# Kernel tuning notes

Measured on AMD Instinct MI355X. Metric: run time of the kernel, lower is better.

The kernel has to match this reference:

```python
import jax, jax.numpy as jnp
import numpy as np

B, L, FD = 16, 196, 2048      # batch, fmap locations (14x14), resnet101 feat dim
N, WD, HD, DD = 1000, 300, 512, 5  # n_class, word_dim, hid_dim, d_dim
E, TMAX, NIMG = 50000, 5, 1000     # n_edges, gru steps, imagenet classes


def setup_inputs():
    key = jax.random.key(0)
    ks = jax.random.split(key, 32)
    p = lambda k, s: (jax.random.normal(k, s, jnp.float32) * 0.02)
    z = lambda n: jnp.zeros((n,), jnp.float32)
    return {
        'feats': jax.random.normal(ks[0], (B, L, FD), jnp.float32),
        'embed': jax.random.normal(ks[1], (N, WD), jnp.float32),
        'edges': jax.random.randint(ks[2], (2, E), 0, N, jnp.int32),
        # attention key/query nets
        'W_key': p(ks[3], (FD, HD)), 'b_key': z(HD),
        'W_query': p(ks[4], (WD, HD)), 'b_query': z(HD),
        # F_in: feat_dim -> 512 -> d_dim (relu)
        'Wf1': p(ks[5], (FD, 512)), 'bf1': z(512),
        'Wf2': p(ks[6], (512, DD)), 'bf2': z(DD),
        # F_rel: 2*word_dim -> 256 -> 1 (relu)
        'Wr1': p(ks[7], (2 * WD, 256)), 'br1': z(256),
        'Wr2': p(ks[8], (256, 1)), 'br2': z(1),
        # F_out: d_dim -> 512 -> 1 (relu)
        'Wo1': p(ks[9], (DD, 512)), 'bo1': z(512),
        'Wo2': p(ks[10], (512, 1)), 'bo2': z(1),
        # GRUCell (torch layout: [3*d, d] stacked r,z,n)
        'W_ih': p(ks[11], (3 * DD, DD)), 'b_ih': z(3 * DD),
        'W_hh': p(ks[12], (3 * DD, DD)), 'b_hh': z(3 * DD),
        # imagenet classifier on pooled features
        'W_clf': p(ks[13], (FD, NIMG)), 'b_clf': z(NIMG),
    }


def _gru_cell(x, h, W_ih, W_hh, b_ih, b_hh):
    gi = x @ W_ih.T + b_ih            # [M, 3d]
    gh = h @ W_hh.T + b_hh
    i_r, i_z, i_n = jnp.split(gi, 3, axis=-1)
    h_r, h_z, h_n = jnp.split(gh, 3, axis=-1)
    r = jax.nn.sigmoid(i_r + h_r)
    zg = jax.nn.sigmoid(i_z + h_z)
    n = jnp.tanh(i_n + r * h_n)
    return (1.0 - zg) * n + zg * h


def reference(feats, embed, edges, W_key, b_key, W_query, b_query,
              Wf1, bf1, Wf2, bf2, Wr1, br1, Wr2, br2, Wo1, bo1, Wo2, bo2,
              W_ih, b_ih, W_hh, b_hh, W_clf, b_clf):
    # imagenet scores from globally pooled backbone features
    pooled = jnp.mean(feats, axis=1)                      # [B, FD]
    imgnet_scores = jax.nn.softmax(pooled @ W_clf + b_clf, axis=1)

    # label-conditional spatial attention
    keys = feats @ W_key + b_key                          # [B, L, HD]
    queries = embed @ W_query + b_query                   # [N, HD]
    scores = jnp.einsum('blh,nh->bnl', keys, queries)     # [B, N, L]
    attn = jax.nn.softmax(scores, axis=2)
    graph_input = jnp.einsum('bnl,blf->bnf', attn, feats) # [B, N, FD]
    graph_input = graph_input.reshape(-1, FD)             # [B*N, FD]

    # F_in MLP -> initial hidden state
    h0 = jax.nn.relu(graph_input @ Wf1 + bf1) @ Wf2 + bf2  # [B*N, DD]

    # edge weights from word-embedding pairs, scattered into dense [N, N]
    et = jnp.concatenate([embed[edges[0]], embed[edges[1]]], axis=1)  # [E, 2*WD]
    vals = jnp.tanh((jax.nn.relu(et @ Wr1 + br1) @ Wr2 + br2).reshape(-1))
    prop_mat = jnp.zeros((N, N), jnp.float32).at[edges[0], edges[1]].add(vals)

    # t_max message-passing + GRU steps (sequential recurrence)
    def step(hidden, _):
        msg = jnp.tanh(jnp.einsum('nm,bmd->bnd', prop_mat,
                                  hidden.reshape(B, N, DD))).reshape(-1, DD)
        return _gru_cell(msg, hidden, W_ih, W_hh, b_ih, b_hh), None
    hidden, _ = jax.lax.scan(step, h0, None, length=TMAX)

    logits = (jax.nn.relu(hidden @ Wo1 + bo1) @ Wo2 + bo2).reshape(B, N)
    return logits, attn, imgnet_scores
```

## Files before the change

kernel.cpp:

```cpp
#include <hip/hip_runtime.h>
#include <hip/hip_bf16.h>
#include <math.h>

#define B_   16
#define L_   196
#define FD_  2048
#define N_   1000
#define WD_  300
#define HD_  512
#define DD_  5
#define E_   50000
#define TMAX_ 5
#define NIMG_ 1000
#define WDP_ 320
#define LP_  224
#define EKP_ 640

typedef __attribute__((ext_vector_type(8))) short bf16x8;
typedef __attribute__((ext_vector_type(4))) float f32x4;

#define SMEM_MEGA1    24832
#define SMEM_MM_SPLIT 24576
#define SMEM_MM_NS    12288
#define SMEM_PREP     4352

__device__ __forceinline__ short bf_hi(float x) {
    unsigned u = __float_as_uint(x);
    unsigned r = u + 0x7fffu + ((u >> 16) & 1u);
    return (short)(r >> 16);
}
__device__ __forceinline__ float bf2f_(short s) {
    return __uint_as_float(((unsigned)(unsigned short)s) << 16);
}

__device__ __forceinline__ void gl16(const short* g, char* l) {
    __builtin_amdgcn_global_load_lds(
        (const __attribute__((address_space(1))) void*)g,
        (__attribute__((address_space(3))) void*)l, 16, 0, 0);
}

#define OUT_SPLIT 1
#define OUT_SC    2
#define OUT_F1T   3
#define OUT_H0    4

template<int OUTMODE, bool SPLIT>
__device__ __forceinline__ void mm_core(
    char* sm, int bx, int by, int zb,
    const short* __restrict__ Ah, const short* __restrict__ Al,
    const short* __restrict__ Bh, const short* __restrict__ Bl,
    const float* __restrict__ bias, void* __restrict__ C0, void* __restrict__ C1,
    void* __restrict__ C2, const float* __restrict__ W2,
    int M, int N, int K, int kbeg, int kend)
{
    char* AsH = sm;
    char* AsL = sm + 8192;
    char* BsH = sm + (SPLIT ? 16384 : 8192);
    char* BsL = sm + 20480;
    int t = threadIdx.x;
    int lane = t & 63, w = t >> 6;
    int q = lane >> 4, r = lane & 15;
    int row0 = by * 128, col0 = bx * 64;

    int srow = t >> 2, cd = t & 3;
    int cg = cd ^ ((srow >> 1) & 3);
    int gA0 = row0 + srow;       if (gA0 >= M) gA0 = M - 1;
    int gA1 = row0 + 64 + srow;  if (gA1 >= M) gA1 = M - 1;
    int gB  = col0 + srow;       if (gB  >= N) gB  = N - 1;
    const short* pA0 = Ah + (long)gA0 * K + cg * 8 + kbeg;
    const short* pA1 = Ah + (long)gA1 * K + cg * 8 + kbeg;
    const short* pB  = Bh + (long)gB  * K + cg * 8 + kbeg;
    const short* pA0l = Ah; const short* pA1l = Ah; const short* pBl = Bh;
    if (SPLIT) {
        pA0l = Al + (long)gA0 * K + cg * 8 + kbeg;
        pA1l = Al + (long)gA1 * K + cg * 8 + kbeg;
        pBl  = Bl + (long)gB  * K + cg * 8 + kbeg;
    }
    char* dA0 = AsH + t * 16;
    char* dA1 = AsH + 4096 + t * 16;
    char* dB  = BsH + t * 16;
    char* dA0l = AsL + t * 16;
    char* dA1l = AsL + 4096 + t * 16;
    char* dBl  = BsL + t * 16;

    int x = (q ^ ((r >> 1) & 3)) * 16;
    int aoff0 = (w * 32 + r) * 64 + x;
    int aoff1 = aoff0 + 1024;
    int boff[4];
    #pragma unroll
    for (int ct = 0; ct < 4; ct++) boff[ct] = (ct * 16 + r) * 64 + x;

    f32x4 zero4 = {0.f, 0.f, 0.f, 0.f};
    f32x4 acc[2][4];
    #pragma unroll
    for (int i = 0; i < 2; i++)
        #pragma unroll
        for (int j = 0; j < 4; j++) acc[i][j] = zero4;

    int nk = (kend - kbeg) >> 5;
    for (int ks = 0; ks < nk; ks++) {
        int ko = ks * 32;
        gl16(pA0 + ko, dA0);
        gl16(pA1 + ko, dA1);
        gl16(pB  + ko, dB);
        if (SPLIT) {
            gl16(pA0l + ko, dA0l);
            gl16(pA1l + ko, dA1l);
            gl16(pBl  + ko, dBl);
        }
        __syncthreads();

        bf16x8 ah0 = *(const bf16x8*)(AsH + aoff0);
        bf16x8 ah1 = *(const bf16x8*)(AsH + aoff1);
        bf16x8 al0, al1;
        if (SPLIT) {
            al0 = *(const bf16x8*)(AsL + aoff0);
            al1 = *(const bf16x8*)(AsL + aoff1);
        }
        #pragma unroll
        for (int ct = 0; ct < 4; ct++) {
            bf16x8 bh = *(const bf16x8*)(BsH + boff[ct]);
            acc[0][ct] = __builtin_amdgcn_mfma_f32_16x16x32_bf16(ah0, bh, acc[0][ct], 0, 0, 0);
            acc[1][ct] = __builtin_amdgcn_mfma_f32_16x16x32_bf16(ah1, bh, acc[1][ct], 0, 0, 0);
            if (SPLIT) {
                acc[0][ct] = __builtin_amdgcn_mfma_f32_16x16x32_bf16(al0, bh, acc[0][ct], 0, 0, 0);
                acc[1][ct] = __builtin_amdgcn_mfma_f32_16x16x32_bf16(al1, bh, acc[1][ct], 0, 0, 0);
                bf16x8 bl = *(const bf16x8*)(BsL + boff[ct]);
                acc[0][ct] = __builtin_amdgcn_mfma_f32_16x16x32_bf16(ah0, bl, acc[0][ct], 0, 0, 0);
                acc[1][ct] = __builtin_amdgcn_mfma_f32_16x16x32_bf16(ah1, bl, acc[1][ct], 0, 0, 0);
            }
        }
        __syncthreads();
    }

    if (OUTMODE == OUT_H0) {
        float s[2][4][DD_];
        #pragma unroll
        for (int i = 0; i < 2; i++)
            #pragma unroll
            for (int reg = 0; reg < 4; reg++)
                #pragma unroll
                for (int d = 0; d < DD_; d++) s[i][reg][d] = 0.f;
        #pragma unroll
        for (int i = 0; i < 2; i++) {
            #pragma unroll
            for (int ct = 0; ct < 4; ct++) {
                int n = col0 + ct * 16 + r;
                float w2v[DD_];
                #pragma unroll
                for (int d = 0; d < DD_; d++) w2v[d] = W2[n * DD_ + d];
                float b1 = bias[n];
                #pragma unroll
                for (int reg = 0; reg < 4; reg++) {
                    int m = row0 + w * 32 + i * 16 + q * 4 + reg;
                    if (m >= M) continue;
                    float val = fmaxf(acc[i][ct][reg] + b1, 0.f);
                    #pragma unroll
                    for (int d = 0; d < DD_; d++) s[i][reg][d] = fmaf(val, w2v[d], s[i][reg][d]);
                }
            }
        }
        #pragma unroll
        for (int i = 0; i < 2; i++)
            #pragma unroll
            for (int reg = 0; reg < 4; reg++)
                #pragma unroll
                for (int d = 0; d < DD_; d++) {
                    float v = s[i][reg][d];
                    v += __shfl_xor(v, 1);
                    v += __shfl_xor(v, 2);
                    v += __shfl_xor(v, 4);
                    v += __shfl_xor(v, 8);
                    if (r == 0) {
                        int m = row0 + w * 32 + i * 16 + q * 4 + reg;
                        if (m < M)
                            atomicAdd(&((float*)C0)[(long)m * (B_ * DD_) + zb * DD_ + d], v);
                    }
                }
        return;
    }

    #pragma unroll
    for (int i = 0; i < 2; i++) {
        #pragma unroll
        for (int ct = 0; ct < 4; ct++) {
            #pragma unroll
            for (int reg = 0; reg < 4; reg++) {
                int m = row0 + w * 32 + i * 16 + q * 4 + reg;
                int n = col0 + ct * 16 + r;
                if (m >= M || n >= N) continue;
                float v = acc[i][ct][reg];
                if (OUTMODE == OUT_SC) {
                    ((float*)C0)[(long)m * N + n] = v;
                } else if (OUTMODE == OUT_F1T) {
                    int b = m / 196, l = m - b * 196;
                    ((short*)C2)[((long)b * 512 + n) * LP_ + l] = bf_hi(v);
                } else {
                    float v2 = v + bias[n];
                    long idx = (long)m * N + n;
                    short hi = bf_hi(v2);
                    ((short*)C0)[idx] = hi;
                    ((short*)C1)[idx] = bf_hi(v2 - bf2f_(hi));
                }
            }
        }
    }
}

__device__ __forceinline__ void edge_core(
    char* sm, int be,
    const short* __restrict__ embedH, const int* __restrict__ edges,
    const short* __restrict__ Wr1T, const float* __restrict__ br1,
    const float* __restrict__ Wr2, const float* __restrict__ br2,
    float* __restrict__ prop)
{
    char* As = sm;
    char* Bs = sm + 4096;
    int* src = (int*)(sm + 20480);
    int* dst = (int*)(sm + 20736);
    float (*part)[5] = (float(*)[5])(sm + 20992);
    int t = threadIdx.x;
    int e0 = be * 64;
    if (t < 64) {
        int e = e0 + t;
        src[t] = (e < E_) ? edges[e] : 0;
        dst[t] = (e < E_) ? edges[E_ + e] : 0;
    }
    __syncthreads();
    int lane = t & 63, w = t >> 6, q = lane >> 4, r = lane & 15;
    f32x4 zero4 = {0.f, 0.f, 0.f, 0.f};
    f32x4 acc[4][4];
    #pragma unroll
    for (int i = 0; i < 4; i++)
        #pragma unroll
        for (int j = 0; j < 4; j++) acc[i][j] = zero4;

    int srow = t >> 2, cd = t & 3;
    int cg = cd ^ ((srow >> 1) & 3);
    const short* baseS = embedH + (long)src[srow] * WDP_ + cg * 8;
    const short* baseD = embedH + (long)dst[srow] * WDP_ + cg * 8;
    const short* pB = Wr1T + (long)srow * EKP_ + cg * 8;
    char* dA = As + t * 16;
    char* dB = Bs + t * 16;

    int x = (q ^ ((r >> 1) & 3)) * 16;
    int aoff[4], boff[4];
    #pragma unroll
    for (int i = 0; i < 4; i++) {
        aoff[i] = (i * 16 + r) * 64 + x;
        boff[i] = (w * 64 + i * 16 + r) * 64 + x;
    }

    for (int ks = 0; ks < 20; ks++) {
        const short* pa = (ks < 10) ? baseS + ks * 32 : baseD + (ks - 10) * 32;
        gl16(pa, dA);
        #pragma unroll
        for (int i = 0; i < 4; i++)
            gl16(pB + (long)i * 64 * EKP_ + ks * 32, dB + i * 4096);
        __syncthreads();

        bf16x8 af[4], bfr[4];
        #pragma unroll
        for (int rt = 0; rt < 4; rt++) af[rt] = *(const bf16x8*)(As + aoff[rt]);
        #pragma unroll
        for (int ct = 0; ct < 4; ct++) bfr[ct] = *(const bf16x8*)(Bs + boff[ct]);
        #pragma unroll
        for (int rt = 0; rt < 4; rt++)
            #pragma unroll
            for (int ct = 0; ct < 4; ct++)
                acc[rt][ct] = __builtin_amdgcn_mfma_f32_16x16x32_bf16(af[rt], bfr[ct], acc[rt][ct], 0, 0, 0);
        __syncthreads();
    }
    float b1v[4], w2v[4];
    #pragma unroll
    for (int ct = 0; ct < 4; ct++) {
        int u = w * 64 + ct * 16 + r;
        b1v[ct] = br1[u];
        w2v[ct] = Wr2[u];
    }
    #pragma unroll
    for (int rt = 0; rt < 4; rt++) {
        #pragma unroll
        for (int reg = 0; reg < 4; reg++) {
            float s = 0.f;
            #pragma unroll
            for (int ct = 0; ct < 4; ct++)
                s = fmaf(fmaxf(acc[rt][ct][reg] + b1v[ct], 0.f), w2v[ct], s);
            s += __shfl_xor(s, 1);
            s += __shfl_xor(s, 2);
            s += __shfl_xor(s, 4);
            s += __shfl_xor(s, 8);
            if (r == 0) part[rt * 16 + q * 4 + reg][w] = s;
        }
    }
    __syncthreads();
    if (t < 64 && e0 + t < E_) {
        float s = part[t][0] + part[t][1] + part[t][2] + part[t][3];
        atomicAdd(&prop[(long)src[t] * N_ + dst[t]], tanhf(s + br2[0]));
    }
}

__device__ __forceinline__ void transconv_core(
    char* sm, int bx, int by,
    const float* __restrict__ in, short* __restrict__ outH, short* __restrict__ outL,
    int Kd, int N, int Ks)
{
    float (*tile)[33] = (float(*)[33])sm;
    int k0 = bx * 32, n0 = by * 32;
    int t = threadIdx.x;
    int tr = t >> 5, tc = t & 31;
    #pragma unroll
    for (int i = 0; i < 4; i++) {
        int k = k0 + tr + i * 8, n = n0 + tc;
        tile[tr + i * 8][tc] = (k < Kd && n < N) ? in[(long)k * N + n] : 0.f;
    }
    __syncthreads();
    #pragma unroll
    for (int i = 0; i < 4; i++) {
        int n = n0 + tr + i * 8, k = k0 + tc;
        if (n < N && k < Ks) {
            float x = tile[tc][tr + i * 8];
            short hi = bf_hi(x);
            outH[(long)n * Ks + k] = hi;
            if (outL) outL[(long)n * Ks + k] = bf_hi(x - bf2f_(hi));
        }
    }
}

__global__ __launch_bounds__(256) void prep(
    float* __restrict__ prop, float* __restrict__ Ht0, const float* __restrict__ bf2,
    const float* __restrict__ feats, float* __restrict__ pooled,
    short* __restrict__ featsH, short* __restrict__ featsL,
    const float* __restrict__ embed, short* __restrict__ embH, short* __restrict__ embL,
    const float* __restrict__ W_key, const float* __restrict__ Wf1,
    short* __restrict__ WkfH, short* __restrict__ WkfL,
    const float* __restrict__ W_query, short* __restrict__ WqTh, short* __restrict__ WqTl,
    const float* __restrict__ Wr1, short* __restrict__ Wr1T, short* __restrict__ F1T)
{
    __shared__ __align__(16) char sm[SMEM_PREP];
    int b = blockIdx.x, t = threadIdx.x;
    if (b < 977) {
        int i = (b * 256 + t) * 4;
        if (i < N_ * N_) { float4 z = {0.f, 0.f, 0.f, 0.f}; *(float4*)(prop + i) = z; }
    } else if (b < 1290) {
        int i = (b - 977) * 256 + t;
        if (i < N_ * B_ * DD_) Ht0[i] = bf2[i % DD_];
    } else if (b < 1418) {
        int idx = (b - 1290) * 256 + t;
        int bb = idx / FD_, f = idx % FD_;
        const float* p = feats + (long)bb * L_ * FD_ + f;
        float acc = 0.f;
        for (int l = 0; l < L_; l++) acc += p[(long)l * FD_];
        pooled[idx] = acc * (1.0f / L_);
    } else if (b < 4554) {
        long i = ((long)(b - 1418) * 256 + t) * 8;
        float4 v0 = *(const float4*)(feats + i);
        float4 v1 = *(const float4*)(feats + i + 4);
        float xs[8] = {v0.x, v0.y, v0.z, v0.w, v1.x, v1.y, v1.z, v1.w};
        short h[8], l8[8];
        #pragma unroll
        for (int j = 0; j < 8; j++) {
            h[j] = bf_hi(xs[j]);
            l8[j] = bf_hi(xs[j] - bf2f_(h[j]));
        }
        *(int4*)(featsH + i) = *(int4*)h;
        *(int4*)(featsL + i) = *(int4*)l8;
    } else if (b < 4867) {
        int i = ((b - 4554) * 256 + t) * 4;
        if (i < N_ * WDP_) {
            int n = i / WDP_, c = i - n * WDP_;
            short h[4], l4[4];
            if (c < WD_) {
                float4 v = *(const float4*)(embed + (long)n * WD_ + c);
                float xs[4] = {v.x, v.y, v.z, v.w};
                #pragma unroll
                for (int j = 0; j < 4; j++) {
                    h[j] = bf_hi(xs[j]);
                    l4[j] = bf_hi(xs[j] - bf2f_(h[j]));
                }
            } else {
                #pragma unroll
                for (int j = 0; j < 4; j++) { h[j] = 0; l4[j] = 0; }
            }
            *(int2*)(embH + (long)n * WDP_ + c) = *(int2*)h;
            *(int2*)(embL + (long)n * WDP_ + c) = *(int2*)l4;
        }
    } else if (b < 5891) {
        int bb = b - 4867;
        transconv_core(sm, bb % 64, bb / 64, W_key, WkfH, WkfL, FD_, HD_, FD_);
    } else if (b < 6915) {
        int bb = b - 5891;
        transconv_core(sm, bb % 64, bb / 64, Wf1, WkfH + (size_t)512 * FD_, nullptr, FD_, HD_, FD_);
    } else if (b < 7075) {
        int bb = b - 6915;
        transconv_core(sm, bb % 10, bb / 10, W_query, WqTh, WqTl, WD_, HD_, WDP_);
    } else if (b < 7235) {
        int bb = b - 7075;
        int bx = bb % 20, by = bb / 20;
        float (*tile)[33] = (float(*)[33])sm;
        int k0 = bx * 32, n0 = by * 32;
        int tr = t >> 5, tc = t & 31;
        #pragma unroll
        for (int i = 0; i < 4; i++) {
            int kout = k0 + tr + i * 8, n = n0 + tc;
            int kin = (kout < 320) ? kout : kout - 20;
            bool valid = (kout < 320) ? (kout < 300) : (kout < 620);
            tile[tr + i * 8][tc] = valid ? Wr1[(long)kin * 256 + n] : 0.f;
        }
        __syncthreads();
        #pragma unroll
        for (int i = 0; i < 4; i++) {
            int n = n0 + tr + i * 8, k = k0 + tc;
            Wr1T[(long)n * EKP_ + k] = bf_hi(tile[tc][tr + i * 8]);
        }
    } else {
        long i = ((long)(b - 7235) * 256 + t) * 8;
        int4 z = {0, 0, 0, 0};
        *(int4*)(F1T + i) = z;
    }
}

__global__ __launch_bounds__(256) void mega1(
    const short* __restrict__ featsH, const short* __restrict__ featsL,
    const short* __restrict__ WkfH, const short* __restrict__ WkfL,
    const float* __restrict__ b_key, short* __restrict__ keysH, short* __restrict__ keysL,
    short* __restrict__ F1T,
    const short* __restrict__ embH, const short* __restrict__ embL,
    const short* __restrict__ WqTh, const short* __restrict__ WqTl,
    const float* __restrict__ b_query, short* __restrict__ qH, short* __restrict__ qL,
    const int* __restrict__ edges, const short* __restrict__ Wr1T,
    const float* __restrict__ br1, const float* __restrict__ Wr2,
    const float* __restrict__ br2, float* __restrict__ prop,
    const float* __restrict__ pooled, const float* __restrict__ W_clf,
    const float* __restrict__ b_clf, float* __restrict__ Pimg)
{
    __shared__ __align__(16) char sm[SMEM_MEGA1];
    int b = blockIdx.x;
    if (b < 200) {
        int l = (b & 7) * 25 + (b >> 3);
        mm_core<OUT_SPLIT, true>(sm, l & 7, l >> 3, 0,
            featsH, featsL, WkfH, WkfL, b_key,
            keysH, keysL, nullptr, nullptr, B_ * L_, 512, FD_, 0, FD_);
    } else if (b < 400) {
        int bb = b - 200;
        int l = (bb & 7) * 25 + (bb >> 3);
        mm_core<OUT_F1T, false>(sm, l & 7, l >> 3, 0,
            featsH, nullptr, WkfH + (size_t)512 * FD_, nullptr, nullptr,
            nullptr, nullptr, F1T, nullptr, B_ * L_, 512, FD_, 0, FD_);
    } else if (b < 464) {
        int bb = b - 400;
        int l = (bb & 7) * 8 + (bb >> 3);
        mm_core<OUT_SPLIT, true>(sm, l & 7, l >> 3, 0,
            embH, embL, WqTh, WqTl, b_query,
            qH, qL, nullptr, nullptr, N_, HD_, WDP_, 0, WDP_);
    } else if (b < 1246) {
        edge_core(sm, b - 464, embH, edges, Wr1T, br1, Wr2, br2, prop);
    } else {
        int bb = b - 1246;
        int ks = bb / 63, ix = bb % 63;
        int i = ix * 256 + threadIdx.x;
        if (i < B_ * NIMG_) {
            int bi = i / NIMG_, n = i % NIMG_;
            const float* p = pooled + (long)bi * FD_ + ks * 256;
            const float* w = W_clf + (long)(ks * 256) * NIMG_ + n;
            float acc = (ks == 0) ? b_clf[n] : 0.f;
            #pragma unroll 4
            for (int k = 0; k < 256; k++) acc = fmaf(p[k], w[(long)k * NIMG_], acc);
            Pimg[(long)ks * (B_ * NIMG_) + i] = acc;
        }
    }
}

__global__ __launch_bounds__(256) void mega2(
    const short* __restrict__ qH, const short* __restrict__ qL,
    const short* __restrict__ keysH, const short* __restrict__ keysL,
    float* __restrict__ Pattn,
    const float* __restrict__ Pimg, float* __restrict__ out_img)
{
    __shared__ __align__(16) char sm[SMEM_MM_SPLIT];
    int b = blockIdx.x;
    if (b < 1024) {
        int l = (b & 7) * 128 + (b >> 3);
        int zb = l >> 6, by = (l >> 3) & 7, kc = (l >> 2) & 1, bx = l & 3;
        const short* Bh = keysH + (long)zb * L_ * HD_;
        const short* Bl = keysL + (long)zb * L_ * HD_;
        float* C0 = Pattn + (long)kc * ((long)B_ * N_ * L_) + (long)zb * N_ * L_;
        mm_core<OUT_SC, true>(sm, bx, by, 0, qH, qL, Bh, Bl, nullptr,
                              C0, nullptr, nullptr, nullptr,
                              N_, L_, HD_, kc * 256, kc * 256 + 256);
    } else {
        int t = threadIdx.x;
        int wave = (b - 1024) * 4 + (t >> 6), lane = t & 63;
        if (wave >= B_) return;
        const int PER = (NIMG_ + 63) / 64;
        float v[PER];
        float m = -1e30f;
        int cnt = 0;
        for (int k = lane; k < NIMG_; k += 64) {
            float s = 0.f;
            #pragma unroll
            for (int ks = 0; ks < 8; ks++) s += Pimg[(long)ks * (B_ * NIMG_) + wave * NIMG_ + k];
            v[cnt] = s; m = fmaxf(m, s); cnt++;
        }
        #pragma unroll
        for (int off = 32; off; off >>= 1) m = fmaxf(m, __shfl_xor(m, off));
        float s = 0.f;
        for (int i = 0; i < cnt; i++) { v[i] = expf(v[i] - m); s += v[i]; }
        #pragma unroll
        for (int off = 32; off; off >>= 1) s += __shfl_xor(s, off);
        float inv = 1.f / s;
        cnt = 0;
        for (int k = lane; k < NIMG_; k += 64) out_img[(long)wave * NIMG_ + k] = v[cnt++] * inv;
    }
}

__global__ void softmax_attn(const float* __restrict__ P0, const float* __restrict__ P1,
                             float* __restrict__ X, short* __restrict__ Xb, int rows)
{
    int gid = blockIdx.x * blockDim.x + threadIdx.x;
    int wave = gid >> 6, lane = gid & 63;
    if (wave >= rows) return;
    const int PER = (L_ + 63) / 64;
    float v[PER];
    float m = -1e30f;
    int cnt = 0;
    for (int k = lane; k < L_; k += 64) {
        long idx = (long)wave * L_ + k;
        v[cnt] = P0[idx] + P1[idx];
        m = fmaxf(m, v[cnt]); cnt++;
    }
    #pragma unroll
    for (int off = 32; off; off >>= 1) m = fmaxf(m, __shfl_xor(m, off));
    float s = 0.f;
    for (int i = 0; i < cnt; i++) { v[i] = expf(v[i] - m); s += v[i]; }
    #pragma unroll
    for (int off = 32; off; off >>= 1) s += __shfl_xor(s, off);
    float inv = 1.f / s;
    cnt = 0;
    for (int k = lane; k < L_; k += 64) {
        float val = v[cnt++] * inv;
        X[(long)wave * L_ + k] = val;
        Xb[(long)wave * LP_ + k] = bf_hi(val);
    }
    if (lane < LP_ - L_) Xb[(long)wave * LP_ + L_ + lane] = 0;
}

__global__ __launch_bounds__(256) void h0gemm(
    const short* __restrict__ attnH, const short* __restrict__ F1T,
    const float* __restrict__ bf1, const float* __restrict__ Wf2,
    float* __restrict__ Ht0)
{
    __shared__ __align__(16) char sm[SMEM_MM_NS];
    int b = blockIdx.x;
    int l = (b & 7) * 128 + (b >> 3);
    int zb = l >> 6, by = (l >> 3) & 7, bx = l & 7;
    const short* Ap = attnH + (long)zb * N_ * LP_;
    const short* Bp = F1T + (long)zb * HD_ * LP_;
    mm_core<OUT_H0, false>(sm, bx, by, zb, Ap, nullptr, Bp, nullptr,
                           bf1, Ht0, nullptr, nullptr, Wf2,
                           N_, HD_, LP_, 0, LP_);
}

__global__ __launch_bounds__(320) void step_kernel(
    const float* __restrict__ prop, const float* __restrict__ Hin,
    float* __restrict__ Hout,
    const float* __restrict__ W_ih, const float* __restrict__ b_ih,
    const float* __restrict__ W_hh, const float* __restrict__ b_hh)
{
    __shared__ float msg[4][80];
    int t = threadIdx.x;
    int nl = t / 80, c = t - nl * 80;
    int n = blockIdx.x * 4 + nl;
    const float* pr = prop + (long)n * N_;
    const float* hc = Hin + c;
    float acc = 0.f;
    #pragma unroll 4
    for (int m4 = 0; m4 < N_; m4 += 4) {
        float4 pv = *(const float4*)(pr + m4);
        acc = fmaf(pv.x, hc[(long)(m4 + 0) * 80], acc);
        acc = fmaf(pv.y, hc[(long)(m4 + 1) * 80], acc);
        acc = fmaf(pv.z, hc[(long)(m4 + 2) * 80], acc);
        acc = fmaf(pv.w, hc[(long)(m4 + 3) * 80], acc);
    }
    msg[nl][c] = tanhf(acc);
    __syncthreads();
    if (t < 64) {
        int nl2 = t >> 4, b = t & 15;
        int n2 = blockIdx.x * 4 + nl2;
        float xv[DD_], h[DD_];
        #pragma unroll
        for (int j = 0; j < DD_; j++) {
            xv[j] = msg[nl2][b * DD_ + j];
            h[j] = Hin[(long)n2 * 80 + b * DD_ + j];
        }
        float gi[3 * DD_], gh[3 * DD_];
        #pragma unroll
        for (int g = 0; g < 3 * DD_; g++) {
            float a = b_ih[g], cc = b_hh[g];
            #pragma unroll
            for (int k = 0; k < DD_; k++) {
                a = fmaf(xv[k], W_ih[g * DD_ + k], a);
                cc = fmaf(h[k], W_hh[g * DD_ + k], cc);
            }
            gi[g] = a; gh[g] = cc;
        }
        #pragma unroll
        for (int j = 0; j < DD_; j++) {
            float rr = 1.f / (1.f + expf(-(gi[j] + gh[j])));
            float zz = 1.f / (1.f + expf(-(gi[DD_ + j] + gh[DD_ + j])));
            float nn2 = tanhf(gi[2 * DD_ + j] + rr * gh[2 * DD_ + j]);
            Hout[(long)n2 * 80 + b * DD_ + j] = (1.f - zz) * nn2 + zz * h[j];
        }
    }
}

__global__ void out_kernel(const float* __restrict__ ht, const float* __restrict__ Wo1,
                           const float* __restrict__ bo1, const float* __restrict__ Wo2,
                           const float* __restrict__ bo2, float* __restrict__ logits, int rows)
{
    int gid = blockIdx.x * blockDim.x + threadIdx.x;
    int wave = gid >> 6, lane = gid & 63;
    if (wave >= rows) return;
    int b = wave / N_, n = wave % N_;
    float x[DD_];
    #pragma unroll
    for (int i = 0; i < DD_; i++) x[i] = ht[(long)n * (B_ * DD_) + b * DD_ + i];
    float acc = 0.f;
    for (int j = lane; j < HD_; j += 64) {
        float h = bo1[j];
        #pragma unroll
        for (int d = 0; d < DD_; d++) h = fmaf(x[d], Wo1[d * HD_ + j], h);
        h = fmaxf(h, 0.f);
        acc = fmaf(h, Wo2[j], acc);
    }
    #pragma unroll
    for (int off = 32; off; off >>= 1) acc += __shfl_down(acc, off);
    if (lane == 0) logits[wave] = acc + bo2[0];
}

extern "C" void kernel_launch(void* const* d_in, const int* in_sizes, int n_in,
                              void* d_out, int out_size, void* d_ws, size_t ws_size,
                              hipStream_t stream)
{
    const float* feats   = (const float*)d_in[0];
    const float* embed   = (const float*)d_in[1];
    const int*   edges   = (const int*)  d_in[2];
    const float* W_key   = (const float*)d_in[3];
    const float* b_key   = (const float*)d_in[4];
    const float* W_query = (const float*)d_in[5];
    const float* b_query = (const float*)d_in[6];
    const float* Wf1     = (const float*)d_in[7];
    const float* bf1     = (const float*)d_in[8];
    const float* Wf2     = (const float*)d_in[9];
    const float* bf2     = (const float*)d_in[10];
    const float* Wr1     = (const float*)d_in[11];
    const float* br1     = (const float*)d_in[12];
    const float* Wr2     = (const float*)d_in[13];
    const float* br2     = (const float*)d_in[14];
    const float* Wo1     = (const float*)d_in[15];
    const float* bo1     = (const float*)d_in[16];
    const float* Wo2     = (const float*)d_in[17];
    const float* bo2     = (const float*)d_in[18];
    const float* W_ih    = (const float*)d_in[19];
    const float* b_ih    = (const float*)d_in[20];
    const float* W_hh    = (const float*)d_in[21];
    const float* b_hh    = (const float*)d_in[22];
    const float* W_clf   = (const float*)d_in[23];
    const float* b_clf   = (const float*)d_in[24];

    float* out_logits = (float*)d_out;
    float* out_attn   = out_logits + B_ * N_;
    float* out_img    = out_attn + (long)B_ * N_ * L_;

    char* p = (char*)d_ws;
    auto alloc = [&](size_t bytes) { void* r = (void*)p; p += (bytes + 255) & ~(size_t)255; return r; };
    float* pooled  = (float*)alloc((size_t)B_ * FD_ * 4);
    short* featsH  = (short*)alloc((size_t)B_ * L_ * FD_ * 2);
    short* featsL  = (short*)alloc((size_t)B_ * L_ * FD_ * 2);
    short* WkfH    = (short*)alloc((size_t)1024 * FD_ * 2);
    short* WkfL    = (short*)alloc((size_t)512 * FD_ * 2);
    short* WqTh    = (short*)alloc((size_t)HD_ * WDP_ * 2);
    short* WqTl    = (short*)alloc((size_t)HD_ * WDP_ * 2);
    short* Wr1T    = (short*)alloc((size_t)256 * EKP_ * 2);
    short* embH    = (short*)alloc((size_t)N_ * WDP_ * 2);
    short* embL    = (short*)alloc((size_t)N_ * WDP_ * 2);
    short* keysH   = (short*)alloc((size_t)B_ * L_ * HD_ * 2);
    short* keysL   = (short*)alloc((size_t)B_ * L_ * HD_ * 2);
    short* qH      = (short*)alloc((size_t)N_ * HD_ * 2);
    short* qL      = (short*)alloc((size_t)N_ * HD_ * 2);
    short* attnH   = (short*)alloc((size_t)B_ * N_ * LP_ * 2);
    short* F1T     = (short*)alloc((size_t)B_ * HD_ * LP_ * 2);
    float* prop    = (float*)alloc((size_t)N_ * N_ * 4);
    float* Ht0     = (float*)alloc((size_t)N_ * B_ * DD_ * 4);
    float* Ht1     = (float*)alloc((size_t)N_ * B_ * DD_ * 4);
    float* Pimg    = (float*)alloc((size_t)8 * B_ * NIMG_ * 4);
    float* Pattn   = (float*)alloc((size_t)2 * B_ * N_ * L_ * 4);

    prep<<<8131, 256, 0, stream>>>(prop, Ht0, bf2, feats, pooled, featsH, featsL,
                                   embed, embH, embL, W_key, Wf1, WkfH, WkfL,
                                   W_query, WqTh, WqTl, Wr1, Wr1T, F1T);

    mega1<<<1750, 256, 0, stream>>>(featsH, featsL, WkfH, WkfL, b_key, keysH, keysL, F1T,
                                    embH, embL, WqTh, WqTl, b_query, qH, qL,
                                    edges, Wr1T, br1, Wr2, br2, prop,
                                    pooled, W_clf, b_clf, Pimg);

    mega2<<<1028, 256, 0, stream>>>(qH, qL, keysH, keysL, Pattn, Pimg, out_img);

    softmax_attn<<<(B_ * N_ * 64 + 255) / 256, 256, 0, stream>>>(
        Pattn, Pattn + (long)B_ * N_ * L_, out_attn, attnH, B_ * N_);

    h0gemm<<<1024, 256, 0, stream>>>(attnH, F1T, bf1, Wf2, Ht0);

    {
        float* hin = Ht0;
        float* hout = Ht1;
        for (int step = 0; step < TMAX_; step++) {
            step_kernel<<<N_ / 4, 320, 0, stream>>>(prop, hin, hout,
                                                    W_ih, b_ih, W_hh, b_hh);
            float* tmp = hin; hin = hout; hout = tmp;
        }
        out_kernel<<<(B_ * N_ * 64 + 255) / 256, 256, 0, stream>>>(hin, Wo1, bo1, Wo2, bo2,
                                                                   out_logits, B_ * N_);
    }
}
```

Baseline: 538.2 us.

## Double-buffer LDS tiles in GEMM and edge-MLP cores with async prefetch

Converts the matmul core and the edge-MLP core from single-buffered LDS staging to ping-pong double buffering. The next K-slice is issued via global_load_lds before computing on the current one, with explicit vmcnt waits and raw s_barrier replacing __syncthreads. This aims to hide global-load latency behind MFMA work. In exchange the LDS footprint doubles, which may reduce occupancy, and the hand-coded waitcnt counts must exactly match the number of loads issued per stage.

```diff
diff --git a/kernel.cpp b/kernel.cpp
--- a/kernel.cpp
+++ b/kernel.cpp
@@ -19,10 +19,13 @@
 typedef __attribute__((ext_vector_type(8))) short bf16x8;
 typedef __attribute__((ext_vector_type(4))) float f32x4;
 
-#define SMEM_MEGA1    24832
-#define SMEM_MM_SPLIT 24576
-#define SMEM_MM_NS    12288
+#define SMEM_MEGA1    49152
+#define SMEM_MM_SPLIT 49152
+#define SMEM_MM_NS    24576
 #define SMEM_PREP     4352
+
+#define SBAR()    asm volatile("s_barrier" ::: "memory")
+#define WVM(N)    asm volatile("s_waitcnt vmcnt(" #N ")" ::: "memory")
 
 __device__ __forceinline__ short bf_hi(float x) {
     unsigned u = __float_as_uint(x);
@@ -53,6 +56,7 @@
     void* __restrict__ C2, const float* __restrict__ W2,
     int M, int N, int K, int kbeg, int kend)
 {
+    const int PBUF = SPLIT ? 24576 : 12288;
     char* AsH = sm;
     char* AsL = sm + 8192;
     char* BsH = sm + (SPLIT ? 16384 : 8192);
@@ -97,40 +101,52 @@
         #pragma unroll
         for (int j = 0; j < 4; j++) acc[i][j] = zero4;
 
+    auto stage = [&](int ks) {
+        int off = (ks & 1) * PBUF;
+        int ko = ks * 32;
+        gl16(pA0 + ko, dA0 + off);
+        gl16(pA1 + ko, dA1 + off);
+        gl16(pB  + ko, dB  + off);
+        if (SPLIT) {
+            gl16(pA0l + ko, dA0l + off);
+            gl16(pA1l + ko, dA1l + off);
+            gl16(pBl  + ko, dBl  + off);
+        }
+    };
+
     int nk = (kend - kbeg) >> 5;
+    stage(0);
     for (int ks = 0; ks < nk; ks++) {
-        int ko = ks * 32;
-        gl16(pA0 + ko, dA0);
-        gl16(pA1 + ko, dA1);
-        gl16(pB  + ko, dB);
-        if (SPLIT) {
-            gl16(pA0l + ko, dA0l);
-            gl16(pA1l + ko, dA1l);
-            gl16(pBl  + ko, dBl);
-        }
-        __syncthreads();
-
-        bf16x8 ah0 = *(const bf16x8*)(AsH + aoff0);
-        bf16x8 ah1 = *(const bf16x8*)(AsH + aoff1);
+        if (ks + 1 < nk) {
+            stage(ks + 1);
+            if (SPLIT) { WVM(6); } else { WVM(3); }
+        } else {
+            WVM(0);
+        }
+        SBAR();
+
+        int cur = (ks & 1) * PBUF;
+        bf16x8 ah0 = *(const bf16x8*)(AsH + cur + aoff0);
+        bf16x8 ah1 = *(const bf16x8*)(AsH + cur + aoff1);
         bf16x8 al0, al1;
         if (SPLIT) {
-            al0 = *(const bf16x8*)(AsL + aoff0);
-            al1 = *(const bf16x8*)(AsL + aoff1);
+            al0 = *(const bf16x8*)(AsL + cur + aoff0);
+            al1 = *(const bf16x8*)(AsL + cur + aoff1);
         }
         #pragma unroll
         for (int ct = 0; ct < 4; ct++) {
-            bf16x8 bh = *(const bf16x8*)(BsH + boff[ct]);
+            bf16x8 bh = *(const bf16x8*)(BsH + cur + boff[ct]);
             acc[0][ct] = __builtin_amdgcn_mfma_f32_16x16x32_bf16(ah0, bh, acc[0][ct], 0, 0, 0);
             acc[1][ct] = __builtin_amdgcn_mfma_f32_16x16x32_bf16(ah1, bh, acc[1][ct], 0, 0, 0);
             if (SPLIT) {
                 acc[0][ct] = __builtin_amdgcn_mfma_f32_16x16x32_bf16(al0, bh, acc[0][ct], 0, 0, 0);
                 acc[1][ct] = __builtin_amdgcn_mfma_f32_16x16x32_bf16(al1, bh, acc[1][ct], 0, 0, 0);
-                bf16x8 bl = *(const bf16x8*)(BsL + boff[ct]);
+                bf16x8 bl = *(const bf16x8*)(BsL + cur + boff[ct]);
                 acc[0][ct] = __builtin_amdgcn_mfma_f32_16x16x32_bf16(ah0, bl, acc[0][ct], 0, 0, 0);
                 acc[1][ct] = __builtin_amdgcn_mfma_f32_16x16x32_bf16(ah1, bl, acc[1][ct], 0, 0, 0);
             }
         }
-        __syncthreads();
+        if (ks + 1 < nk) SBAR();
     }
 
     if (OUTMODE == OUT_H0) {
@@ -214,11 +230,12 @@
     const float* __restrict__ Wr2, const float* __restrict__ br2,
     float* __restrict__ prop)
 {
+    const int EPBUF = 20480;
     char* As = sm;
     char* Bs = sm + 4096;
-    int* src = (int*)(sm + 20480);
-    int* dst = (int*)(sm + 20736);
-    float (*part)[5] = (float(*)[5])(sm + 20992);
+    int* src = (int*)(sm + 40960);
+    int* dst = (int*)(sm + 41216);
+    float (*part)[5] = (float(*)[5])(sm + 41472);
     int t = threadIdx.x;
     int e0 = be * 64;
     if (t < 64) {
@@ -251,25 +268,37 @@
         boff[i] = (w * 64 + i * 16 + r) * 64 + x;
     }
 
+    auto estage = [&](int ks) {
+        int off = (ks & 1) * EPBUF;
+        const short* pa = (ks < 10) ? baseS + ks * 32 : baseD + (ks - 10) * 32;
+        gl16(pa, dA + off);
+        #pragma unroll
+        for (int i = 0; i < 4; i++)
+            gl16(pB + (long)i * 64 * EKP_ + ks * 32, dB + i * 4096 + off);
+    };
+
+    estage(0);
     for (int ks = 0; ks < 20; ks++) {
-        const short* pa = (ks < 10) ? baseS + ks * 32 : baseD + (ks - 10) * 32;
-        gl16(pa, dA);
-        #pragma unroll
-        for (int i = 0; i < 4; i++)
-            gl16(pB + (long)i * 64 * EKP_ + ks * 32, dB + i * 4096);
-        __syncthreads();
-
+        if (ks + 1 < 20) {
+            estage(ks + 1);
+            WVM(5);
+        } else {
+            WVM(0);
+        }
+        SBAR();
+
+        int cur = (ks & 1) * EPBUF;
         bf16x8 af[4], bfr[4];
         #pragma unroll
-        for (int rt = 0; rt < 4; rt++) af[rt] = *(const bf16x8*)(As + aoff[rt]);
-        #pragma unroll
-        for (int ct = 0; ct < 4; ct++) bfr[ct] = *(const bf16x8*)(Bs + boff[ct]);
+        for (int rt = 0; rt < 4; rt++) af[rt] = *(const bf16x8*)(As + cur + aoff[rt]);
+        #pragma unroll
+        for (int ct = 0; ct < 4; ct++) bfr[ct] = *(const bf16x8*)(Bs + cur + boff[ct]);
         #pragma unroll
         for (int rt = 0; rt < 4; rt++)
             #pragma unroll
             for (int ct = 0; ct < 4; ct++)
                 acc[rt][ct] = __builtin_amdgcn_mfma_f32_16x16x32_bf16(af[rt], bfr[ct], acc[rt][ct], 0, 0, 0);
-        __syncthreads();
+        if (ks + 1 < 20) SBAR();
     }
     float b1v[4], w2v[4];
     #pragma unroll
```

Measured after the change: 524.0 us. -2.6%, faster.
